# Performance work log

Hardware: AMD Instinct MI355X
Metric: run time of the kernel (lower is better)

The kernel has to match this reference:

```python
import jax, jax.numpy as jnp
import numpy as np
import math

N_FREQ = 50
ENC_DIM = 4 * N_FREQ  # 200
D = 5
N_GENES = 1000
N_CELLS = 5000
N_FRAG = 200_000


def sine_encoding(coords):
    # frequencies: [f1,f1,f2,f2,...] length 2*N_FREQ; shifts: [0, pi/2, 0, pi/2, ...]
    i = jnp.arange(1, N_FREQ + 1, dtype=jnp.float32)
    freqs = jnp.repeat(1.0 / jnp.power(jnp.float32(1000.0), 2.0 * i / N_FREQ), 2)
    shifts = jnp.tile(jnp.array([0.0, math.pi / 2], jnp.float32), N_FREQ)
    # coords [F,2] -> [F,2,2*nf] -> [F,4*nf]
    return jnp.sin((coords[..., None] * freqs + shifts).reshape(coords.shape[0], -1))


def self_attention(x):
    # x: [G, i, D]; NOTE: scale uses sqrt(seq_len) = sqrt(x.shape[-2]) as in the original
    scores = jnp.einsum('gid,gjd->gij', x, x) / jnp.sqrt(jnp.float32(x.shape[1]))
    w = jax.nn.softmax(scores, axis=-1)
    return jnp.einsum('gij,gjd->gid', w, x)


def setup_inputs() -> dict:
    key = jax.random.key(0)
    ks = jax.random.split(key, 6)
    coordinates = jax.random.uniform(ks[0], (N_FRAG, 2), jnp.float32, -1000.0, 1000.0)
    genemapping = jax.random.randint(ks[1], (N_FRAG,), 0, N_GENES)
    local_cellxgene_ix = jax.random.randint(ks[2], (N_FRAG,), 0, N_CELLS * N_GENES)
    genes_oi = jnp.arange(N_GENES)
    # ragged groups: disjoint fragment index sets for group sizes 2, 3, 4
    n2 = jnp.arange(60000)             # 30000 pairs
    n3 = jnp.arange(60000) + 60000     # 20000 triples
    n4 = jnp.arange(60000) + 120000    # 15000 quads
    stdv = 1.0 / math.sqrt(D)
    weight1_frag = jax.random.uniform(ks[3], (N_GENES, ENC_DIM, D), jnp.float32, -stdv, stdv)
    weight1_expr = jnp.ones((N_GENES, D), jnp.float32)
    bias1 = jax.random.normal(ks[4], (N_GENES,), jnp.float32)  # mean_gene_expression
    return dict(coordinates=coordinates, genemapping=genemapping, n2=n2, n3=n3, n4=n4,
                local_cellxgene_ix=local_cellxgene_ix, genes_oi=genes_oi,
                weight1_frag=weight1_frag, weight1_expr=weight1_expr, bias1=bias1)


def reference(coordinates, genemapping, n2, n3, n4, local_cellxgene_ix, genes_oi,
              weight1_frag, weight1_expr, bias1):
    # FragmentEmbedder: sine encode, per-gene weight gather, contract, sigmoid
    enc = sine_encoding(coordinates)                                 # [F, 200]
    emb = jax.nn.sigmoid(jnp.einsum('fe,fed->fd', enc, weight1_frag[genemapping]))  # [F, 5]
    # ragged self-attention over fixed-size groups (2, 3, 4)
    for idx, i in ((n2, 2), (n3, 3), (n4, 4)):
        x = emb[idx].reshape(-1, i, D)
        emb = emb.at[idx].set(self_attention(x).reshape(-1, D))
    # EmbeddingGenePooler: segment sum over cell x gene
    pooled = jax.ops.segment_sum(emb, local_cellxgene_ix, num_segments=N_CELLS * N_GENES)
    cell_gene_embedding = pooled.reshape(N_CELLS, N_GENES, D)
    # EmbeddingToExpression: gene-wise weighted sum + mean expression bias
    return (cell_gene_embedding * weight1_expr[genes_oi]).sum(-1) + bias1[genes_oi]
```

## Files before the change

kernel.cpp:

```cpp
#include <hip/hip_runtime.h>
#include <math.h>

#define DD 5
#define NFREQ 50
#define NB 128

__global__ __launch_bounds__(256) void hist_init_kernel(
    const int* __restrict__ gm, int F, int chunk,
    int* __restrict__ bc, int n_genes, int* __restrict__ done,
    unsigned char* __restrict__ mask,
    float* __restrict__ out, const float* __restrict__ bias,
    const int* __restrict__ genes_oi, int total4) {
  __shared__ int cnt[1000];
  const int gtid = blockIdx.x * blockDim.x + threadIdx.x;
  const int gs = gridDim.x * blockDim.x;
  if (gtid == 0) *done = 0;
  int F4 = F >> 2;
  int* mask4 = (int*)mask;
  for (int i = gtid; i < F4; i += gs) mask4[i] = 0;
  for (int i = (F4 << 2) + gtid; i < F; i += gs) mask[i] = 0;
  for (int v4 = gtid; v4 < total4; v4 += gs) {
    int idx = v4 * 4;
    int j = idx % n_genes;
    float4 vv;
    vv.x = bias[genes_oi[j + 0]];
    vv.y = bias[genes_oi[j + 1]];
    vv.z = bias[genes_oi[j + 2]];
    vv.w = bias[genes_oi[j + 3]];
    reinterpret_cast<float4*>(out)[v4] = vv;
  }
  if (blockIdx.x < NB) {
    for (int j = threadIdx.x; j < n_genes; j += blockDim.x) cnt[j] = 0;
    __syncthreads();
    int b = blockIdx.x;
    int lo = b * chunk;
    int hi = min(F, lo + chunk);
    for (int i = lo + threadIdx.x; i < hi; i += blockDim.x)
      atomicAdd(&cnt[gm[i]], 1);
    __syncthreads();
    for (int j = threadIdx.x; j < n_genes; j += blockDim.x)
      bc[j * NB + b] = cnt[j];
  }
}

__global__ __launch_bounds__(256) void binscan_starts_kernel(
    int* __restrict__ bc, int n_genes, int* __restrict__ totals,
    int* __restrict__ starts, int* __restrict__ done, int nblocks,
    unsigned char* __restrict__ mask,
    const int* __restrict__ n2, int c2,
    const int* __restrict__ n3, int c3,
    const int* __restrict__ n4, int c4) {
  __shared__ int s_amlast;
  __shared__ int s_ws[4];
  const int gtid = blockIdx.x * blockDim.x + threadIdx.x;
  const int gs = gridDim.x * blockDim.x;
  int lane = threadIdx.x & 63;
  int wv = threadIdx.x >> 6;
  int bin = blockIdx.x * 4 + wv;
  if (bin < n_genes) {
    int2* row = (int2*)(bc + (size_t)bin * NB);
    int2 v = row[lane];
    int p = v.x + v.y;
    int ip = p;
#pragma unroll
    for (int off = 1; off < 64; off <<= 1) {
      int q = __shfl_up(ip, off);
      if (lane >= off) ip += q;
    }
    int base = ip - p;
    int2 e;
    e.x = base;
    e.y = base + v.x;
    row[lane] = e;
    if (lane == 63) totals[bin] = ip;
  }
  for (int i = gtid; i < c2; i += gs) mask[n2[i]] = 1;
  for (int i = gtid; i < c3; i += gs) mask[n3[i]] = 1;
  for (int i = gtid; i < c4; i += gs) mask[n4[i]] = 1;
  __syncthreads();
  if (threadIdx.x == 0) {
    __threadfence();
    int tk = atomicAdd(done, 1);
    s_amlast = (tk == nblocks - 1);
  }
  __syncthreads();
  if (!s_amlast) return;
  __threadfence();
  int t = threadIdx.x;
  int4 v = make_int4(0, 0, 0, 0);
  if (4 * t < n_genes) v = ((const int4*)totals)[t];
  int p = v.x + v.y + v.z + v.w;
  int ip = p;
#pragma unroll
  for (int off = 1; off < 64; off <<= 1) {
    int q = __shfl_up(ip, off);
    if (lane >= off) ip += q;
  }
  if (lane == 63) s_ws[wv] = ip;
  __syncthreads();
  int add = 0;
#pragma unroll
  for (int i = 0; i < 4; ++i)
    if (i < wv) add += s_ws[i];
  int excl = add + ip - p;
  int4 e;
  e.x = excl;
  e.y = excl + v.x;
  e.z = e.y + v.y;
  e.w = e.z + v.z;
  if (4 * t < n_genes) ((int4*)starts)[t] = e;
  if (4 * t + 4 == n_genes) starts[n_genes] = e.w + v.w;
}

__global__ __launch_bounds__(256) void blockscatter_kernel(
    const int* __restrict__ gm, int F, int chunk,
    const int* __restrict__ bc, const int* __restrict__ starts,
    int* __restrict__ order, int n_genes) {
  __shared__ int cur[1000];
  int b = blockIdx.x;
  for (int j = threadIdx.x; j < n_genes; j += blockDim.x)
    cur[j] = starts[j] + bc[j * NB + b];
  __syncthreads();
  int lo = b * chunk;
  int hi = min(F, lo + chunk);
  for (int i = lo + threadIdx.x; i < hi; i += blockDim.x) {
    int g = gm[i];
    int p = atomicAdd(&cur[g], 1);
    order[p] = i;
  }
}

__global__ __launch_bounds__(256) void embed_kernel(
    const float2* __restrict__ coords, const int* __restrict__ order,
    const int* __restrict__ starts, const float* __restrict__ W,
    float* __restrict__ emb) {
  __shared__ float s_freq[NFREQ];
  if (threadIdx.x < NFREQ)
    s_freq[threadIdx.x] = exp2f(-0.39863137f * (float)(threadIdx.x + 1));
  __syncthreads();
  int g = blockIdx.x;
  int s0 = starts[g];
  int s1 = starts[g + 1];
  const float* __restrict__ Wg = W + (size_t)g * (4 * NFREQ * DD);

  for (int i = s0 + threadIdx.x; i < s1; i += blockDim.x) {
    int f = order[i];
    float2 xy = coords[f];
    float a0 = 0.f, a1 = 0.f, a2 = 0.f, a3 = 0.f, a4 = 0.f;
    for (int k = 0; k < NFREQ; ++k) {
      float fr = s_freq[k];
      float ax = xy.x * fr;
      float ay = xy.y * fr;
      float sx = __sinf(ax), cx = __cosf(ax);
      float sy = __sinf(ay), cy = __cosf(ay);
      const float* w0s = Wg + (2 * k) * DD;
      const float* w0c = w0s + DD;
      const float* w1s = Wg + (2 * NFREQ + 2 * k) * DD;
      const float* w1c = w1s + DD;
      a0 += sx * w0s[0] + cx * w0c[0] + sy * w1s[0] + cy * w1c[0];
      a1 += sx * w0s[1] + cx * w0c[1] + sy * w1s[1] + cy * w1c[1];
      a2 += sx * w0s[2] + cx * w0c[2] + sy * w1s[2] + cy * w1c[2];
      a3 += sx * w0s[3] + cx * w0c[3] + sy * w1s[3] + cy * w1c[3];
      a4 += sx * w0s[4] + cx * w0c[4] + sy * w1s[4] + cy * w1c[4];
    }
    float* e = emb + (size_t)f * DD;
    e[0] = 1.f / (1.f + __expf(-a0));
    e[1] = 1.f / (1.f + __expf(-a1));
    e[2] = 1.f / (1.f + __expf(-a2));
    e[3] = 1.f / (1.f + __expf(-a3));
    e[4] = 1.f / (1.f + __expf(-a4));
  }
}

template <int SZ>
__device__ __forceinline__ void attn_group_pool(const int* __restrict__ idx,
                                                const float* __restrict__ emb,
                                                const int* __restrict__ lci,
                                                const int* __restrict__ genes_oi,
                                                const float* __restrict__ wexpr,
                                                int n_genes, float* __restrict__ out) {
  int fid[SZ];
  float x[SZ][DD];
#pragma unroll
  for (int a = 0; a < SZ; ++a) {
    fid[a] = idx[a];
    const float* p = emb + (size_t)fid[a] * DD;
#pragma unroll
    for (int d = 0; d < DD; ++d) x[a][d] = p[d];
  }
  const float scale = rsqrtf((float)SZ);
#pragma unroll
  for (int a = 0; a < SZ; ++a) {
    float sc[SZ];
    float m = -1e30f;
#pragma unroll
    for (int b = 0; b < SZ; ++b) {
      float dt = 0.f;
#pragma unroll
      for (int d = 0; d < DD; ++d) dt += x[a][d] * x[b][d];
      sc[b] = dt * scale;
      m = fmaxf(m, sc[b]);
    }
    float sum = 0.f;
#pragma unroll
    for (int b = 0; b < SZ; ++b) {
      sc[b] = __expf(sc[b] - m);
      sum += sc[b];
    }
    float inv = 1.f / sum;
    int ix = lci[fid[a]];
    int g = genes_oi[ix % n_genes];
    const float* w = wexpr + (size_t)g * DD;
    float s = 0.f;
#pragma unroll
    for (int d = 0; d < DD; ++d) {
      float acc = 0.f;
#pragma unroll
      for (int b = 0; b < SZ; ++b) acc += sc[b] * x[b][d];
      s += acc * w[d];
    }
    atomicAdd(out + ix, s * inv);
  }
}

__global__ __launch_bounds__(256) void attn_pool_kernel(
    const int* __restrict__ n2, int g2,
    const int* __restrict__ n3, int g3,
    const int* __restrict__ n4, int g4,
    const float* __restrict__ emb, const int* __restrict__ lci,
    const int* __restrict__ genes_oi, const float* __restrict__ wexpr,
    const unsigned char* __restrict__ mask,
    int F, int n_genes, float* __restrict__ out) {
  int gtid = blockIdx.x * blockDim.x + threadIdx.x;
  int gs = gridDim.x * blockDim.x;
  int gtot = g2 + g3 + g4;
  for (int w = gtid; w < gtot; w += gs) {
    if (w < g2)
      attn_group_pool<2>(n2 + (size_t)w * 2, emb, lci, genes_oi, wexpr, n_genes, out);
    else if (w < g2 + g3)
      attn_group_pool<3>(n3 + (size_t)(w - g2) * 3, emb, lci, genes_oi, wexpr, n_genes, out);
    else
      attn_group_pool<4>(n4 + (size_t)(w - g2 - g3) * 4, emb, lci, genes_oi, wexpr, n_genes, out);
  }
  for (int f = gtid; f < F; f += gs) {
    if (mask[f]) continue;
    int ix = lci[f];
    int g = genes_oi[ix % n_genes];
    const float* e = emb + (size_t)f * DD;
    const float* w = wexpr + (size_t)g * DD;
    float s = e[0] * w[0] + e[1] * w[1] + e[2] * w[2] + e[3] * w[3] + e[4] * w[4];
    atomicAdd(out + ix, s);
  }
}

extern "C" void kernel_launch(void* const* d_in, const int* in_sizes, int n_in,
                              void* d_out, int out_size, void* d_ws, size_t ws_size,
                              hipStream_t stream) {
  const float2* coords  = (const float2*)d_in[0];
  const int* gm         = (const int*)d_in[1];
  const int* n2         = (const int*)d_in[2];
  const int* n3         = (const int*)d_in[3];
  const int* n4         = (const int*)d_in[4];
  const int* lci        = (const int*)d_in[5];
  const int* genes_oi   = (const int*)d_in[6];
  const float* W        = (const float*)d_in[7];
  const float* wexpr    = (const float*)d_in[8];
  const float* bias     = (const float*)d_in[9];
  float* out            = (float*)d_out;

  const int F       = in_sizes[1];
  const int n_genes = in_sizes[6];
  const int c2 = in_sizes[2];
  const int c3 = in_sizes[3];
  const int c4 = in_sizes[4];
  const int g2 = c2 / 2;
  const int g3 = c3 / 3;
  const int g4 = c4 / 4;

  char* ws = (char*)d_ws;
  size_t off = 0;
  float* emb   = (float*)(ws + off); off += (size_t)F * DD * sizeof(float);
  int* order   = (int*)(ws + off);   off += (size_t)F * sizeof(int);
  int* bc      = (int*)(ws + off);   off += (size_t)n_genes * NB * sizeof(int);
  off = (off + 15) & ~(size_t)15;
  int* starts  = (int*)(ws + off);   off += (size_t)(n_genes + 4) * sizeof(int);
  off = (off + 15) & ~(size_t)15;
  int* totals  = (int*)(ws + off);   off += (size_t)n_genes * sizeof(int);
  int* done    = (int*)(ws + off);   off += 4 * sizeof(int);
  off = (off + 15) & ~(size_t)15;
  unsigned char* mask = (unsigned char*)(ws + off); off += (size_t)F;

  const int tb = 256;
  const int chunk = (F + NB - 1) / NB;
  const int total4 = out_size / 4;

  hist_init_kernel<<<1024, tb, 0, stream>>>(gm, F, chunk, bc, n_genes, done,
                                            mask, out, bias, genes_oi, total4);
  int scan_blocks = (n_genes + 3) / 4;
  binscan_starts_kernel<<<scan_blocks, tb, 0, stream>>>(bc, n_genes, totals,
                                                        starts, done, scan_blocks,
                                                        mask, n2, c2, n3, c3, n4, c4);
  blockscatter_kernel<<<NB, tb, 0, stream>>>(gm, F, chunk, bc, starts, order, n_genes);
  embed_kernel<<<n_genes, tb, 0, stream>>>(coords, order, starts, W, emb);
  attn_pool_kernel<<<1250, tb, 0, stream>>>(n2, g2, n3, g3, n4, g4,
                                            emb, lci, genes_oi, wexpr,
                                            mask, F, n_genes, out);
}
```

Baseline: 142.9 us.

## Fuse bin scan into scatter, drop fragment mask via delta pooling, pad embeddings

The separate scan kernel and its last-block atomic handshake are removed. Each scatter block now recomputes the global gene totals and its own block prefix from a block-major count table, then scatters directly. The mask over grouped fragments is eliminated: every fragment pools its raw embedding, and attention groups add the difference between the attended and raw embedding. Embeddings are padded to a stride of 8 floats so they can be read and written with float4, and the pool grid shrinks to 1024 blocks. The cost is redundant count-table reads in each scatter block and extra atomics, since grouped fragments now contribute twice.

```diff
diff --git a/kernel.cpp b/kernel.cpp
--- a/kernel.cpp
+++ b/kernel.cpp
@@ -2,23 +2,30 @@
 #include <math.h>
 
 #define DD 5
+#define EST 8
 #define NFREQ 50
 #define NB 128
 
 __global__ __launch_bounds__(256) void hist_init_kernel(
     const int* __restrict__ gm, int F, int chunk,
-    int* __restrict__ bc, int n_genes, int* __restrict__ done,
-    unsigned char* __restrict__ mask,
+    int* __restrict__ bc, int n_genes,
     float* __restrict__ out, const float* __restrict__ bias,
     const int* __restrict__ genes_oi, int total4) {
   __shared__ int cnt[1000];
   const int gtid = blockIdx.x * blockDim.x + threadIdx.x;
   const int gs = gridDim.x * blockDim.x;
-  if (gtid == 0) *done = 0;
-  int F4 = F >> 2;
-  int* mask4 = (int*)mask;
-  for (int i = gtid; i < F4; i += gs) mask4[i] = 0;
-  for (int i = (F4 << 2) + gtid; i < F; i += gs) mask[i] = 0;
+  if (blockIdx.x < NB) {
+    for (int j = threadIdx.x; j < n_genes; j += blockDim.x) cnt[j] = 0;
+    __syncthreads();
+    int lo = blockIdx.x * chunk;
+    int hi = min(F, lo + chunk);
+    for (int i = lo + threadIdx.x; i < hi; i += blockDim.x)
+      atomicAdd(&cnt[gm[i]], 1);
+    __syncthreads();
+    int* dst = bc + (size_t)blockIdx.x * n_genes;
+    for (int j = threadIdx.x; j < n_genes; j += blockDim.x)
+      dst[j] = cnt[j];
+  }
   for (int v4 = gtid; v4 < total4; v4 += gs) {
     int idx = v4 * 4;
     int j = idx % n_genes;
@@ -29,66 +36,43 @@
     vv.w = bias[genes_oi[j + 3]];
     reinterpret_cast<float4*>(out)[v4] = vv;
   }
-  if (blockIdx.x < NB) {
-    for (int j = threadIdx.x; j < n_genes; j += blockDim.x) cnt[j] = 0;
-    __syncthreads();
-    int b = blockIdx.x;
-    int lo = b * chunk;
-    int hi = min(F, lo + chunk);
-    for (int i = lo + threadIdx.x; i < hi; i += blockDim.x)
-      atomicAdd(&cnt[gm[i]], 1);
-    __syncthreads();
-    for (int j = threadIdx.x; j < n_genes; j += blockDim.x)
-      bc[j * NB + b] = cnt[j];
-  }
-}
-
-__global__ __launch_bounds__(256) void binscan_starts_kernel(
-    int* __restrict__ bc, int n_genes, int* __restrict__ totals,
-    int* __restrict__ starts, int* __restrict__ done, int nblocks,
-    unsigned char* __restrict__ mask,
-    const int* __restrict__ n2, int c2,
-    const int* __restrict__ n3, int c3,
-    const int* __restrict__ n4, int c4) {
-  __shared__ int s_amlast;
+}
+
+__global__ __launch_bounds__(256) void scatter_kernel(
+    const int* __restrict__ gm, int F, int chunk,
+    const int* __restrict__ bc, int n_genes,
+    int* __restrict__ order, int* __restrict__ starts) {
+  __shared__ int s_tot[1024];
+  __shared__ int s_pref[1000];
+  __shared__ int s_cur[1000];
   __shared__ int s_ws[4];
-  const int gtid = blockIdx.x * blockDim.x + threadIdx.x;
-  const int gs = gridDim.x * blockDim.x;
-  int lane = threadIdx.x & 63;
-  int wv = threadIdx.x >> 6;
-  int bin = blockIdx.x * 4 + wv;
-  if (bin < n_genes) {
-    int2* row = (int2*)(bc + (size_t)bin * NB);
-    int2 v = row[lane];
-    int p = v.x + v.y;
-    int ip = p;
-#pragma unroll
-    for (int off = 1; off < 64; off <<= 1) {
-      int q = __shfl_up(ip, off);
-      if (lane >= off) ip += q;
-    }
-    int base = ip - p;
-    int2 e;
-    e.x = base;
-    e.y = base + v.x;
-    row[lane] = e;
-    if (lane == 63) totals[bin] = ip;
-  }
-  for (int i = gtid; i < c2; i += gs) mask[n2[i]] = 1;
-  for (int i = gtid; i < c3; i += gs) mask[n3[i]] = 1;
-  for (int i = gtid; i < c4; i += gs) mask[n4[i]] = 1;
-  __syncthreads();
-  if (threadIdx.x == 0) {
-    __threadfence();
-    int tk = atomicAdd(done, 1);
-    s_amlast = (tk == nblocks - 1);
-  }
-  __syncthreads();
-  if (!s_amlast) return;
-  __threadfence();
-  int t = threadIdx.x;
-  int4 v = make_int4(0, 0, 0, 0);
-  if (4 * t < n_genes) v = ((const int4*)totals)[t];
+  const int tid = threadIdx.x;
+  const int b = blockIdx.x;
+  if (tid < 24) s_tot[1000 + tid] = 0;
+  int tot[4] = {0, 0, 0, 0}, pre[4] = {0, 0, 0, 0};
+  for (int bp = 0; bp < NB; ++bp) {
+    const int* __restrict__ row = bc + (size_t)bp * n_genes;
+#pragma unroll
+    for (int j = 0; j < 4; ++j) {
+      int g = tid + 256 * j;
+      if (g < n_genes) {
+        int v = row[g];
+        tot[j] += v;
+        if (bp < b) pre[j] += v;
+      }
+    }
+  }
+#pragma unroll
+  for (int j = 0; j < 4; ++j) {
+    int g = tid + 256 * j;
+    if (g < n_genes) {
+      s_tot[g] = tot[j];
+      s_pref[g] = pre[j];
+    }
+  }
+  __syncthreads();
+  int lane = tid & 63, wv = tid >> 6;
+  int4 v = ((const int4*)s_tot)[tid];
   int p = v.x + v.y + v.z + v.w;
   int ip = p;
 #pragma unroll
@@ -108,25 +92,23 @@
   e.y = excl + v.x;
   e.z = e.y + v.y;
   e.w = e.z + v.z;
-  if (4 * t < n_genes) ((int4*)starts)[t] = e;
-  if (4 * t + 4 == n_genes) starts[n_genes] = e.w + v.w;
-}
-
-__global__ __launch_bounds__(256) void blockscatter_kernel(
-    const int* __restrict__ gm, int F, int chunk,
-    const int* __restrict__ bc, const int* __restrict__ starts,
-    int* __restrict__ order, int n_genes) {
-  __shared__ int cur[1000];
-  int b = blockIdx.x;
-  for (int j = threadIdx.x; j < n_genes; j += blockDim.x)
-    cur[j] = starts[j] + bc[j * NB + b];
+  if (4 * tid < n_genes) {
+    s_cur[4 * tid + 0] = e.x + s_pref[4 * tid + 0];
+    s_cur[4 * tid + 1] = e.y + s_pref[4 * tid + 1];
+    s_cur[4 * tid + 2] = e.z + s_pref[4 * tid + 2];
+    s_cur[4 * tid + 3] = e.w + s_pref[4 * tid + 3];
+    if (b == 0) {
+      ((int4*)starts)[tid] = e;
+      if (4 * tid + 4 == n_genes) starts[n_genes] = e.w + v.w;
+    }
+  }
   __syncthreads();
   int lo = b * chunk;
   int hi = min(F, lo + chunk);
-  for (int i = lo + threadIdx.x; i < hi; i += blockDim.x) {
+  for (int i = lo + tid; i < hi; i += blockDim.x) {
     int g = gm[i];
-    int p = atomicAdd(&cur[g], 1);
-    order[p] = i;
+    int pos = atomicAdd(&s_cur[g], 1);
+    order[pos] = i;
   }
 }
 
@@ -163,30 +145,33 @@
       a3 += sx * w0s[3] + cx * w0c[3] + sy * w1s[3] + cy * w1c[3];
       a4 += sx * w0s[4] + cx * w0c[4] + sy * w1s[4] + cy * w1c[4];
     }
-    float* e = emb + (size_t)f * DD;
-    e[0] = 1.f / (1.f + __expf(-a0));
-    e[1] = 1.f / (1.f + __expf(-a1));
-    e[2] = 1.f / (1.f + __expf(-a2));
-    e[3] = 1.f / (1.f + __expf(-a3));
+    float* e = emb + (size_t)f * EST;
+    float4 r;
+    r.x = 1.f / (1.f + __expf(-a0));
+    r.y = 1.f / (1.f + __expf(-a1));
+    r.z = 1.f / (1.f + __expf(-a2));
+    r.w = 1.f / (1.f + __expf(-a3));
+    *reinterpret_cast<float4*>(e) = r;
     e[4] = 1.f / (1.f + __expf(-a4));
   }
 }
 
 template <int SZ>
-__device__ __forceinline__ void attn_group_pool(const int* __restrict__ idx,
-                                                const float* __restrict__ emb,
-                                                const int* __restrict__ lci,
-                                                const int* __restrict__ genes_oi,
-                                                const float* __restrict__ wexpr,
-                                                int n_genes, float* __restrict__ out) {
+__device__ __forceinline__ void attn_group_delta(const int* __restrict__ idx,
+                                                 const float* __restrict__ emb,
+                                                 const int* __restrict__ lci,
+                                                 const int* __restrict__ genes_oi,
+                                                 const float* __restrict__ wexpr,
+                                                 int n_genes, float* __restrict__ out) {
   int fid[SZ];
   float x[SZ][DD];
 #pragma unroll
   for (int a = 0; a < SZ; ++a) {
     fid[a] = idx[a];
-    const float* p = emb + (size_t)fid[a] * DD;
-#pragma unroll
-    for (int d = 0; d < DD; ++d) x[a][d] = p[d];
+    const float* p = emb + (size_t)fid[a] * EST;
+    float4 v = *reinterpret_cast<const float4*>(p);
+    x[a][0] = v.x; x[a][1] = v.y; x[a][2] = v.z; x[a][3] = v.w;
+    x[a][4] = p[4];
   }
   const float scale = rsqrtf((float)SZ);
 #pragma unroll
@@ -217,9 +202,9 @@
       float acc = 0.f;
 #pragma unroll
       for (int b = 0; b < SZ; ++b) acc += sc[b] * x[b][d];
-      s += acc * w[d];
-    }
-    atomicAdd(out + ix, s * inv);
+      s += (acc * inv - x[a][d]) * w[d];
+    }
+    atomicAdd(out + ix, s);
   }
 }
 
@@ -229,26 +214,25 @@
     const int* __restrict__ n4, int g4,
     const float* __restrict__ emb, const int* __restrict__ lci,
     const int* __restrict__ genes_oi, const float* __restrict__ wexpr,
-    const unsigned char* __restrict__ mask,
     int F, int n_genes, float* __restrict__ out) {
   int gtid = blockIdx.x * blockDim.x + threadIdx.x;
   int gs = gridDim.x * blockDim.x;
   int gtot = g2 + g3 + g4;
   for (int w = gtid; w < gtot; w += gs) {
     if (w < g2)
-      attn_group_pool<2>(n2 + (size_t)w * 2, emb, lci, genes_oi, wexpr, n_genes, out);
+      attn_group_delta<2>(n2 + (size_t)w * 2, emb, lci, genes_oi, wexpr, n_genes, out);
     else if (w < g2 + g3)
-      attn_group_pool<3>(n3 + (size_t)(w - g2) * 3, emb, lci, genes_oi, wexpr, n_genes, out);
+      attn_group_delta<3>(n3 + (size_t)(w - g2) * 3, emb, lci, genes_oi, wexpr, n_genes, out);
     else
-      attn_group_pool<4>(n4 + (size_t)(w - g2 - g3) * 4, emb, lci, genes_oi, wexpr, n_genes, out);
+      attn_group_delta<4>(n4 + (size_t)(w - g2 - g3) * 4, emb, lci, genes_oi, wexpr, n_genes, out);
   }
   for (int f = gtid; f < F; f += gs) {
-    if (mask[f]) continue;
     int ix = lci[f];
     int g = genes_oi[ix % n_genes];
-    const float* e = emb + (size_t)f * DD;
+    const float* e = emb + (size_t)f * EST;
+    float4 v = *reinterpret_cast<const float4*>(e);
     const float* w = wexpr + (size_t)g * DD;
-    float s = e[0] * w[0] + e[1] * w[1] + e[2] * w[2] + e[3] * w[3] + e[4] * w[4];
+    float s = v.x * w[0] + v.y * w[1] + v.z * w[2] + v.w * w[3] + e[4] * w[4];
     atomicAdd(out + ix, s);
   }
 }
@@ -270,39 +254,27 @@
 
   const int F       = in_sizes[1];
   const int n_genes = in_sizes[6];
-  const int c2 = in_sizes[2];
-  const int c3 = in_sizes[3];
-  const int c4 = in_sizes[4];
-  const int g2 = c2 / 2;
-  const int g3 = c3 / 3;
-  const int g4 = c4 / 4;
+  const int g2 = in_sizes[2] / 2;
+  const int g3 = in_sizes[3] / 3;
+  const int g4 = in_sizes[4] / 4;
 
   char* ws = (char*)d_ws;
   size_t off = 0;
-  float* emb   = (float*)(ws + off); off += (size_t)F * DD * sizeof(float);
+  float* emb   = (float*)(ws + off); off += (size_t)F * EST * sizeof(float);
   int* order   = (int*)(ws + off);   off += (size_t)F * sizeof(int);
-  int* bc      = (int*)(ws + off);   off += (size_t)n_genes * NB * sizeof(int);
+  int* bc      = (int*)(ws + off);   off += (size_t)NB * n_genes * sizeof(int);
   off = (off + 15) & ~(size_t)15;
   int* starts  = (int*)(ws + off);   off += (size_t)(n_genes + 4) * sizeof(int);
-  off = (off + 15) & ~(size_t)15;
-  int* totals  = (int*)(ws + off);   off += (size_t)n_genes * sizeof(int);
-  int* done    = (int*)(ws + off);   off += 4 * sizeof(int);
-  off = (off + 15) & ~(size_t)15;
-  unsigned char* mask = (unsigned char*)(ws + off); off += (size_t)F;
 
   const int tb = 256;
   const int chunk = (F + NB - 1) / NB;
   const int total4 = out_size / 4;
 
-  hist_init_kernel<<<1024, tb, 0, stream>>>(gm, F, chunk, bc, n_genes, done,
-                                            mask, out, bias, genes_oi, total4);
-  int scan_blocks = (n_genes + 3) / 4;
-  binscan_starts_kernel<<<scan_blocks, tb, 0, stream>>>(bc, n_genes, totals,
-                                                        starts, done, scan_blocks,
-                                                        mask, n2, c2, n3, c3, n4, c4);
-  blockscatter_kernel<<<NB, tb, 0, stream>>>(gm, F, chunk, bc, starts, order, n_genes);
+  hist_init_kernel<<<1024, tb, 0, stream>>>(gm, F, chunk, bc, n_genes,
+                                            out, bias, genes_oi, total4);
+  scatter_kernel<<<NB, tb, 0, stream>>>(gm, F, chunk, bc, n_genes, order, starts);
   embed_kernel<<<n_genes, tb, 0, stream>>>(coords, order, starts, W, emb);
-  attn_pool_kernel<<<1250, tb, 0, stream>>>(n2, g2, n3, g3, n4, g4,
+  attn_pool_kernel<<<1024, tb, 0, stream>>>(n2, g2, n3, g3, n4, g4,
                                             emb, lci, genes_oi, wexpr,
-                                            mask, F, n_genes, out);
-}
+                                            F, n_genes, out);
+}
```

After: 260.2 us. 82.0% more time.
